# Kernel optimization log

Hardware: AMD Instinct MI355X
Metric: run time of the kernel (lower is better)

## Reference

```python
import jax, jax.numpy as jnp
import numpy as np

NUM_BINS = 256


def _apply_A(a):
    # sigmoid -> matmul with upper-triangular ones == inclusive cumsum along bins
    a = jax.nn.sigmoid(a)              # [B, 256]
    a = jnp.cumsum(a, axis=1)          # equivalent to a @ triu(ones(256,256))
    # global (whole-tensor) min-max normalization, as in the torch code
    return (a - a.min()) / (a.max() - a.min())


def setup_inputs() -> dict:
    key = jax.random.key(0)
    k1, k2, k3, k4 = jax.random.split(key, 4)
    B, C, H, W = 16, 3, 1024, 1024
    img_low = jax.random.uniform(k1, (B, C, H, W), dtype=jnp.float32)
    rr = jax.random.normal(k2, (B, NUM_BINS), dtype=jnp.float32)
    gr = jax.random.normal(k3, (B, NUM_BINS), dtype=jnp.float32)
    br = jax.random.normal(k4, (B, NUM_BINS), dtype=jnp.float32)
    return {"img_low": img_low, "rr": rr, "gr": gr, "br": br}


def reference(img_low, rr, gr, br):
    B, C, H, W = img_low.shape
    r = _apply_A(rr)
    g = _apply_A(gr)
    b = _apply_A(br)
    curve = jnp.stack([r, g, b], axis=1)  # [B, 3, 256]
    # img.mul(255).clamp(0,255).to(int64): truncation toward zero (floor for >=0)
    idx = jnp.clip(img_low * 255.0, 0.0, 255.0).astype(jnp.int32)  # [B, C, H, W]
    # per-pixel LUT gather: res[b,c,h,w] = curve[b, c, idx[b,c,h,w]]
    flat = jnp.take_along_axis(
        curve.reshape(B * C, NUM_BINS), idx.reshape(B * C, H * W), axis=1
    )
    return flat.reshape(B, C, H, W)
```

## Files before the change

### kernel.cpp

```cpp
#include <hip/hip_runtime.h>
#include <math.h>

#define NUM_BINS 256
#define BATCH 16
#define PLANE_PIX (1024 * 1024)

__device__ __forceinline__ float sigmoidf_(float x) {
    return 1.0f / (1.0f + expf(-x));
}

__global__ __launch_bounds__(256) void curves_kernel(
    const float* __restrict__ rr, const float* __restrict__ gr,
    const float* __restrict__ br, float* __restrict__ curve)
{
    const int ch = blockIdx.x;
    const float* src = (ch == 0) ? rr : (ch == 1) ? gr : br;

    __shared__ float s[BATCH][NUM_BINS];
    __shared__ float s_mn, s_inv;

    const int t = threadIdx.x;

    for (int i = t; i < BATCH * NUM_BINS; i += 256) {
        s[i >> 8][i & 255] = sigmoidf_(src[i]);
    }
    __syncthreads();

    const int wave = t >> 6;
    const int lane = t & 63;
    for (int row = wave; row < BATCH; row += 4) {
        float v0 = s[row][lane * 4 + 0];
        float v1 = s[row][lane * 4 + 1];
        float v2 = s[row][lane * 4 + 2];
        float v3 = s[row][lane * 4 + 3];
        float p1 = v0 + v1;
        float p2 = p1 + v2;
        float p3 = p2 + v3;
        float sum = p3;
        #pragma unroll
        for (int d = 1; d < 64; d <<= 1) {
            float o = __shfl_up(sum, d, 64);
            if (lane >= d) sum += o;
        }
        const float off = sum - p3;
        s[row][lane * 4 + 0] = off + v0;
        s[row][lane * 4 + 1] = off + p1;
        s[row][lane * 4 + 2] = off + p2;
        s[row][lane * 4 + 3] = off + p3;
    }
    __syncthreads();

    if (t == 0) {
        float mn = s[0][0], mx = s[0][NUM_BINS - 1];
        for (int r = 1; r < BATCH; ++r) {
            mn = fminf(mn, s[r][0]);
            mx = fmaxf(mx, s[r][NUM_BINS - 1]);
        }
        s_mn = mn;
        s_inv = 1.0f / (mx - mn);
    }
    __syncthreads();

    const float mn = s_mn;
    const float inv = s_inv;
    for (int i = t; i < BATCH * NUM_BINS; i += 256) {
        const int row = i >> 8, col = i & 255;
        curve[(row * 3 + ch) * NUM_BINS + col] = (s[row][col] - mn) * inv;
    }
}

__global__ __launch_bounds__(256) void lut_kernel(
    const float* __restrict__ img, const float* __restrict__ curve,
    float* __restrict__ out)
{
    __shared__ float lut[NUM_BINS];
    const int plane = blockIdx.y;
    lut[threadIdx.x] = curve[plane * NUM_BINS + threadIdx.x];
    __syncthreads();

    const size_t planeOff = (size_t)plane * PLANE_PIX;
    const float4* __restrict__ src = (const float4*)(img + planeOff);
    float4*       __restrict__ dst = (float4*)(out + planeOff);

    const int base = blockIdx.x * 1024 + threadIdx.x;
    #pragma unroll
    for (int k = 0; k < 4; ++k) {
        const int i = base + k * 256;
        const float4 v = src[i];
        float4 o;
        o.x = lut[(int)fminf(fmaxf(v.x * 255.0f, 0.0f), 255.0f)];
        o.y = lut[(int)fminf(fmaxf(v.y * 255.0f, 0.0f), 255.0f)];
        o.z = lut[(int)fminf(fmaxf(v.z * 255.0f, 0.0f), 255.0f)];
        o.w = lut[(int)fminf(fmaxf(v.w * 255.0f, 0.0f), 255.0f)];
        dst[i] = o;
    }
}

extern "C" void kernel_launch(void* const* d_in, const int* in_sizes, int n_in,
                              void* d_out, int out_size, void* d_ws, size_t ws_size,
                              hipStream_t stream) {
    const float* img = (const float*)d_in[0];
    const float* rr  = (const float*)d_in[1];
    const float* gr  = (const float*)d_in[2];
    const float* br  = (const float*)d_in[3];
    float* out   = (float*)d_out;
    float* curve = (float*)d_ws;

    curves_kernel<<<dim3(3), dim3(256), 0, stream>>>(rr, gr, br, curve);
    lut_kernel<<<dim3(256, 48), dim3(256), 0, stream>>>(img, curve, out);
}
```

Baseline: 82.07 us.

## Fuse curve construction into LUT kernel with per-block redundant min/max computation

Drops the separate curve kernel: every block recomputes the sigmoid cumsum for its own row, plus the global min (first element of each row) and max (row totals via wave reductions) across the 16 rows of its channel. This removes a kernel launch and the serial dependency on a 3-block kernel, at the cost of redundant per-block work reading 16 rows of parameters. It also doubles the per-thread vector work to 8 float4s, which halves the block count, and uses nontemporal stores and the fast __expf intrinsic. The min/max now come from row totals summed in a different order than the cumsum, which can cause small rounding differences.

Result: faster. 65.95 us (-19.6%).

```diff
diff --git a/kernel.cpp b/kernel.cpp
--- a/kernel.cpp
+++ b/kernel.cpp
@@ -4,95 +4,96 @@
 #define NUM_BINS 256
 #define BATCH 16
 #define PLANE_PIX (1024 * 1024)
+#define VEC_PER_PLANE (PLANE_PIX / 4)
+#define F4_PER_THREAD 8
+#define BLOCKS_PER_PLANE (VEC_PER_PLANE / (256 * F4_PER_THREAD))
+
+typedef float f32x4 __attribute__((ext_vector_type(4)));
 
 __device__ __forceinline__ float sigmoidf_(float x) {
-    return 1.0f / (1.0f + expf(-x));
+    return 1.0f / (1.0f + __expf(-x));
 }
 
-__global__ __launch_bounds__(256) void curves_kernel(
+__global__ __launch_bounds__(256) void curve_fused_kernel(
+    const float* __restrict__ img,
     const float* __restrict__ rr, const float* __restrict__ gr,
-    const float* __restrict__ br, float* __restrict__ curve)
+    const float* __restrict__ br, float* __restrict__ out)
 {
-    const int ch = blockIdx.x;
-    const float* src = (ch == 0) ? rr : (ch == 1) ? gr : br;
-
-    __shared__ float s[BATCH][NUM_BINS];
+    __shared__ float srow[NUM_BINS];
+    __shared__ float lut[NUM_BINS];
+    __shared__ float wmax_s[4], wmin_s[4];
     __shared__ float s_mn, s_inv;
 
+    const int plane = blockIdx.y;
+    const int b = plane / 3;
+    const int c = plane - 3 * b;
+    const float* __restrict__ src = (c == 0) ? rr : (c == 1) ? gr : br;
+
     const int t = threadIdx.x;
+    const int wave = t >> 6, lane = t & 63;
 
-    for (int i = t; i < BATCH * NUM_BINS; i += 256) {
-        s[i >> 8][i & 255] = sigmoidf_(src[i]);
+    srow[t] = sigmoidf_(src[b * NUM_BINS + t]);
+
+    float wmax = -1e30f, wmin = 1e30f;
+    for (int r = wave; r < BATCH; r += 4) {
+        const float* __restrict__ row = src + r * NUM_BINS;
+        const float s0 = sigmoidf_(row[lane]);
+        const float s1 = sigmoidf_(row[lane + 64]);
+        const float s2 = sigmoidf_(row[lane + 128]);
+        const float s3 = sigmoidf_(row[lane + 192]);
+        if (lane == 0) wmin = fminf(wmin, s0);
+        float sum = (s0 + s1) + (s2 + s3);
+        #pragma unroll
+        for (int d = 32; d > 0; d >>= 1) sum += __shfl_xor(sum, d, 64);
+        wmax = fmaxf(wmax, sum);
     }
+    if (lane == 0) { wmax_s[wave] = wmax; wmin_s[wave] = wmin; }
     __syncthreads();
 
-    const int wave = t >> 6;
-    const int lane = t & 63;
-    for (int row = wave; row < BATCH; row += 4) {
-        float v0 = s[row][lane * 4 + 0];
-        float v1 = s[row][lane * 4 + 1];
-        float v2 = s[row][lane * 4 + 2];
-        float v3 = s[row][lane * 4 + 3];
-        float p1 = v0 + v1;
-        float p2 = p1 + v2;
-        float p3 = p2 + v3;
+    if (wave == 0) {
+        const float v0 = srow[lane * 4 + 0];
+        const float v1 = srow[lane * 4 + 1];
+        const float v2 = srow[lane * 4 + 2];
+        const float v3 = srow[lane * 4 + 3];
+        const float p1 = v0 + v1, p2 = p1 + v2, p3 = p2 + v3;
         float sum = p3;
         #pragma unroll
         for (int d = 1; d < 64; d <<= 1) {
-            float o = __shfl_up(sum, d, 64);
+            const float o = __shfl_up(sum, d, 64);
             if (lane >= d) sum += o;
         }
         const float off = sum - p3;
-        s[row][lane * 4 + 0] = off + v0;
-        s[row][lane * 4 + 1] = off + p1;
-        s[row][lane * 4 + 2] = off + p2;
-        s[row][lane * 4 + 3] = off + p3;
+        srow[lane * 4 + 0] = off + v0;
+        srow[lane * 4 + 1] = off + p1;
+        srow[lane * 4 + 2] = off + p2;
+        srow[lane * 4 + 3] = off + p3;
+        if (lane == 0) {
+            const float mx = fmaxf(fmaxf(wmax_s[0], wmax_s[1]),
+                                   fmaxf(wmax_s[2], wmax_s[3]));
+            const float mn = fminf(fminf(wmin_s[0], wmin_s[1]),
+                                   fminf(wmin_s[2], wmin_s[3]));
+            s_mn = mn;
+            s_inv = 1.0f / (mx - mn);
+        }
     }
     __syncthreads();
-
-    if (t == 0) {
-        float mn = s[0][0], mx = s[0][NUM_BINS - 1];
-        for (int r = 1; r < BATCH; ++r) {
-            mn = fminf(mn, s[r][0]);
-            mx = fmaxf(mx, s[r][NUM_BINS - 1]);
-        }
-        s_mn = mn;
-        s_inv = 1.0f / (mx - mn);
-    }
+    lut[t] = (srow[t] - s_mn) * s_inv;
     __syncthreads();
 
-    const float mn = s_mn;
-    const float inv = s_inv;
-    for (int i = t; i < BATCH * NUM_BINS; i += 256) {
-        const int row = i >> 8, col = i & 255;
-        curve[(row * 3 + ch) * NUM_BINS + col] = (s[row][col] - mn) * inv;
-    }
-}
-
-__global__ __launch_bounds__(256) void lut_kernel(
-    const float* __restrict__ img, const float* __restrict__ curve,
-    float* __restrict__ out)
-{
-    __shared__ float lut[NUM_BINS];
-    const int plane = blockIdx.y;
-    lut[threadIdx.x] = curve[plane * NUM_BINS + threadIdx.x];
-    __syncthreads();
-
-    const size_t planeOff = (size_t)plane * PLANE_PIX;
-    const float4* __restrict__ src = (const float4*)(img + planeOff);
-    float4*       __restrict__ dst = (float4*)(out + planeOff);
-
-    const int base = blockIdx.x * 1024 + threadIdx.x;
+    const size_t planeOff4 = (size_t)plane * VEC_PER_PLANE;
+    const f32x4* __restrict__ sp = (const f32x4*)img + planeOff4;
+    f32x4* __restrict__ dp = (f32x4*)out + planeOff4;
+    const int base = blockIdx.x * (256 * F4_PER_THREAD) + t;
     #pragma unroll
-    for (int k = 0; k < 4; ++k) {
+    for (int k = 0; k < F4_PER_THREAD; ++k) {
         const int i = base + k * 256;
-        const float4 v = src[i];
-        float4 o;
+        const f32x4 v = sp[i];
+        f32x4 o;
         o.x = lut[(int)fminf(fmaxf(v.x * 255.0f, 0.0f), 255.0f)];
         o.y = lut[(int)fminf(fmaxf(v.y * 255.0f, 0.0f), 255.0f)];
         o.z = lut[(int)fminf(fmaxf(v.z * 255.0f, 0.0f), 255.0f)];
         o.w = lut[(int)fminf(fmaxf(v.w * 255.0f, 0.0f), 255.0f)];
-        dst[i] = o;
+        __builtin_nontemporal_store(o, dp + i);
     }
 }
 
@@ -103,9 +104,8 @@
     const float* rr  = (const float*)d_in[1];
     const float* gr  = (const float*)d_in[2];
     const float* br  = (const float*)d_in[3];
-    float* out   = (float*)d_out;
-    float* curve = (float*)d_ws;
+    float* out = (float*)d_out;
 
-    curves_kernel<<<dim3(3), dim3(256), 0, stream>>>(rr, gr, br, curve);
-    lut_kernel<<<dim3(256, 48), dim3(256), 0, stream>>>(img, curve, out);
+    curve_fused_kernel<<<dim3(BLOCKS_PER_PLANE, 48), dim3(256), 0, stream>>>(
+        img, rr, gr, br, out);
 }
```
